# Kernel optimization log

Measured on AMD Instinct MI355X. Metric: run time of the kernel, lower is better.

The kernel has to match this reference:

```python
import jax, jax.numpy as jnp
import numpy as np

H = 8          # attention heads
HID = 256      # hidden dim
C = HID // H   # per-head channels
N = 50000      # nodes per node type
E = 500000     # edges per edge type
LRELU_SLOPE = 0.2
EPS_SOFTMAX = 1e-16
EPS_LN = 1e-5


def _gat(x_src, x_dst, ei, W, a_s, a_d, b, n_dst):
    # PyG GATConv (shared lin for src/dst since in_channels is int), concat heads
    h_src = (x_src @ W).reshape(-1, H, C)   # (Nsrc, H, C)
    h_dst = (x_dst @ W).reshape(-1, H, C)   # (Ndst, H, C)
    al_s = (h_src * a_s).sum(-1)            # (Nsrc, H)
    al_d = (h_dst * a_d).sum(-1)            # (Ndst, H)
    src, dst = ei[0], ei[1]
    alpha = jax.nn.leaky_relu(al_s[src] + al_d[dst], LRELU_SLOPE)  # (E, H)
    # segment softmax over edges grouped by destination node
    amax = jax.ops.segment_max(alpha, dst, num_segments=n_dst)
    amax = jnp.where(jnp.isfinite(amax), amax, 0.0)
    ex = jnp.exp(alpha - amax[dst])
    den = jax.ops.segment_sum(ex, dst, num_segments=n_dst)
    w = ex / (den[dst] + EPS_SOFTMAX)
    msg = h_src[src] * w[:, :, None]        # (E, H, C)
    out = jax.ops.segment_sum(msg, dst, num_segments=n_dst)
    return out.reshape(n_dst, HID) + b


def _ln(x, g, b):
    mu = x.mean(-1, keepdims=True)
    var = x.var(-1, keepdims=True)
    return (x - mu) / jnp.sqrt(var + EPS_LN) * g + b


def setup_inputs() -> dict:
    key = jax.random.key(0)
    ks = jax.random.split(key, 24)
    s = 1.0 / np.sqrt(HID)
    d = {}
    d["x_gene"] = jax.random.normal(ks[0], (N, HID), jnp.float32)
    d["x_pheno"] = jax.random.normal(ks[1], (N, HID), jnp.float32)
    d["ei_gp"] = jax.random.randint(ks[2], (2, E), 0, N, jnp.int32)
    d["ei_pg"] = jax.random.randint(ks[3], (2, E), 0, N, jnp.int32)
    d["ei_gg"] = jax.random.randint(ks[4], (2, E), 0, N, jnp.int32)
    i = 5
    for tag in ["gp", "pg", "gg"]:
        d[f"W_{tag}"] = jax.random.normal(ks[i], (HID, HID), jnp.float32) * s; i += 1
        d[f"a_s_{tag}"] = jax.random.normal(ks[i], (H, C), jnp.float32) * s; i += 1
        d[f"a_d_{tag}"] = jax.random.normal(ks[i], (H, C), jnp.float32) * s; i += 1
        d[f"b_{tag}"] = jnp.zeros((HID,), jnp.float32); i += 1
    d["ln_g_gene"] = jnp.ones((HID,), jnp.float32)
    d["ln_b_gene"] = jnp.zeros((HID,), jnp.float32)
    d["ln_g_ph"] = jnp.ones((HID,), jnp.float32)
    d["ln_b_ph"] = jnp.zeros((HID,), jnp.float32)
    return d


def reference(x_gene, x_pheno, ei_gp, ei_pg, ei_gg,
              W_gp, a_s_gp, a_d_gp, b_gp,
              W_pg, a_s_pg, a_d_pg, b_pg,
              W_gg, a_s_gg, a_d_gg, b_gg,
              ln_g_gene, ln_b_gene, ln_g_ph, ln_b_ph):
    # HeteroConv aggr='sum': sum conv outputs per destination node type
    out_gene = (_gat(x_pheno, x_gene, ei_pg, W_pg, a_s_pg, a_d_pg, b_pg, N)
                + _gat(x_gene, x_gene, ei_gg, W_gg, a_s_gg, a_d_gg, b_gg, N))
    out_ph = _gat(x_gene, x_pheno, ei_gp, W_gp, a_s_gp, a_d_gp, b_gp, N)
    # residual + layernorm (dropout is identity in eval / p=0)
    out_gene = _ln(out_gene + x_gene, ln_g_gene, ln_b_gene)
    out_ph = _ln(out_ph + x_pheno, ln_g_ph, ln_b_ph)
    return (out_gene, out_ph)
```

## Files before the change

kernel.cpp:

```cpp
#include <hip/hip_runtime.h>

#define NN 50000
#define EE 500000
#define CAP 64

typedef unsigned int u32;
typedef unsigned short ushort;
typedef __attribute__((ext_vector_type(8))) short short8v;
typedef __attribute__((ext_vector_type(4))) float float4v;

__device__ __forceinline__ ushort f2b(float f) {
  u32 u = __float_as_uint(f);
  u32 r = (u + 0x7fffu + ((u >> 16) & 1u)) >> 16;
  return (ushort)r;
}
__device__ __forceinline__ u32 pk2(float a, float b) {
  return (u32)f2b(a) | ((u32)f2b(b) << 16);
}
__device__ __forceinline__ float bl(u32 q) { return __uint_as_float(q << 16); }
__device__ __forceinline__ float bh(u32 q) { return __uint_as_float(q & 0xffff0000u); }
__device__ __forceinline__ void gload16(const void* g, void* l) {
  __builtin_amdgcn_global_load_lds((const __attribute__((address_space(1))) void*)g,
                                   (__attribute__((address_space(3))) void*)l, 16, 0, 0);
}

__global__ void prep_kernel(const float* __restrict__ W_gp, const float* __restrict__ W_pg,
                            const float* __restrict__ W_gg,
                            const float* __restrict__ as_gp, const float* __restrict__ as_pg,
                            const float* __restrict__ as_gg,
                            const float* __restrict__ ad_gp, const float* __restrict__ ad_pg,
                            const float* __restrict__ ad_gg,
                            const float* __restrict__ xg, const float* __restrict__ xp,
                            const int* __restrict__ e0, const int* __restrict__ e1,
                            const int* __restrict__ e2,
                            ushort* __restrict__ WT, ushort* __restrict__ V6T,
                            ushort* __restrict__ xb, int* __restrict__ cnt3,
                            ushort* __restrict__ srcs3) {
  int b = blockIdx.x;
  int k = threadIdx.x;
  if (b < 256) {
    int n = b;
    WT[(size_t)0 * 65536 + n * 256 + k] = f2b(W_gp[k * 256 + n]);
    WT[(size_t)1 * 65536 + n * 256 + k] = f2b(W_pg[k * 256 + n]);
    WT[(size_t)2 * 65536 + n * 256 + k] = f2b(W_gg[k * 256 + n]);
    return;
  }
  if (b < 304) {
    int idx = b - 256;
    int g = idx >> 3, h = idx & 7;
    const float* W;
    const float* a;
    switch (g) {
      case 0: W = W_gp; a = as_gp; break;
      case 1: W = W_gg; a = as_gg; break;
      case 2: W = W_pg; a = ad_pg; break;
      case 3: W = W_gg; a = ad_gg; break;
      case 4: W = W_pg; a = as_pg; break;
      default: W = W_gp; a = ad_gp; break;
    }
    const float4* wrow = (const float4*)&W[(size_t)k * 256 + h * 32];
    const float4* arow = (const float4*)&a[h * 32];
    float s = 0.f;
#pragma unroll
    for (int q = 0; q < 8; ++q) {
      float4 wv = wrow[q];
      float4 av = arow[q];
      s += wv.x * av.x + wv.y * av.y + wv.z * av.z + wv.w * av.w;
    }
    V6T[(size_t)(g * 8 + h) * 256 + k] = f2b(s);
    return;
  }
  if (b == 304) {
#pragma unroll
    for (int col = 48; col < 64; ++col) V6T[(size_t)col * 256 + k] = 0;
    return;
  }
  if (b < 2353) {
    int i = (b - 305) * 256 + k;
    const int gstride = 2048 * 256;
    const int tot = 2 * NN * 64;
    for (; i < tot; i += gstride) {
      const float* src = (i < NN * 64) ? xg + (size_t)i * 4 : xp + ((size_t)i - (size_t)NN * 64) * 4;
      float4 v = *(const float4*)src;
      ushort4 o;
      o.x = f2b(v.x); o.y = f2b(v.y); o.z = f2b(v.z); o.w = f2b(v.w);
      *(ushort4*)&xb[(size_t)i * 4] = o;
    }
    return;
  }
  int i = (b - 2353) * 256 + k;
  if (i >= 3 * EE) return;
  int which = i >= 2 * EE ? 2 : (i >= EE ? 1 : 0);
  const int* ei = which == 0 ? e0 : (which == 1 ? e1 : e2);
  int e = i - which * EE;
  int d = ei[EE + e];
  int s = ei[e];
  int gslot = which * NN + d;
  int pos = atomicAdd(&cnt3[gslot], 1);
  if (pos < CAP) srcs3[(size_t)gslot * CAP + pos] = (ushort)s;
}

__global__ __launch_bounds__(256) void compute_kernel(
    const ushort* __restrict__ xb, const ushort* __restrict__ WT,
    const ushort* __restrict__ V6T, ushort* __restrict__ hb3,
    ushort* __restrict__ alsb, float* __restrict__ ald3) {
  __shared__ ushort smem[16384];
  const int tid = threadIdx.x;
  const int l = tid & 63, w = tid >> 6;
  const int rr = l & 15, kb = l >> 4;
  if (blockIdx.y < 6) {
    ushort* As = smem;
    ushort* Bs = smem + 8192;
    const int yy = blockIdx.y;
    const int p = yy >> 1;
    const int c0 = (yy & 1) * 128;
    const ushort* x = xb + (p == 1 ? (size_t)NN * 256 : 0);
    const ushort* Wp = WT + (size_t)p * 65536 + (size_t)c0 * 256;
    ushort* hb = hb3 + (size_t)p * 12800000;
    const int r0 = blockIdx.x * 128;
    const int wm = w >> 1, wn = w & 1;
    float4v acc[4][4];
#pragma unroll
    for (int mi = 0; mi < 4; ++mi)
#pragma unroll
      for (int ni = 0; ni < 4; ++ni) acc[mi][ni] = (float4v){0.f, 0.f, 0.f, 0.f};
    const int r1 = tid >> 2, g1 = tid & 3;
    const int r2 = 64 + (tid >> 2), g2 = tid & 3;

#define STAGE(buf, k0)                                                               \
  {                                                                                  \
    gload16(&x[(size_t)(r0 + r1) * 256 + (k0) + g1 * 8], &As[(buf) * 4096 + tid * 8]); \
    gload16(&x[(size_t)(r0 + r2) * 256 + (k0) + g2 * 8], &As[(buf) * 4096 + (tid + 256) * 8]); \
    gload16(&Wp[(size_t)r1 * 256 + (k0) + g1 * 8], &Bs[(buf) * 4096 + tid * 8]);     \
    gload16(&Wp[(size_t)r2 * 256 + (k0) + g2 * 8], &Bs[(buf) * 4096 + (tid + 256) * 8]); \
  }

    STAGE(0, 0);
    __syncthreads();
#pragma unroll
    for (int k = 0; k < 8; ++k) {
      const int buf = k & 1;
      if (k < 7) STAGE(buf ^ 1, (k + 1) * 32);
      short8v af[4], bf[4];
#pragma unroll
      for (int t = 0; t < 4; ++t) {
        af[t] = *(const short8v*)&As[buf * 4096 + (wm * 64 + t * 16 + rr) * 32 + kb * 8];
        bf[t] = *(const short8v*)&Bs[buf * 4096 + (wn * 64 + t * 16 + rr) * 32 + kb * 8];
      }
#pragma unroll
      for (int mi = 0; mi < 4; ++mi)
#pragma unroll
        for (int ni = 0; ni < 4; ++ni)
          acc[mi][ni] = __builtin_amdgcn_mfma_f32_16x16x32_bf16(bf[ni], af[mi], acc[mi][ni], 0, 0, 0);
      __syncthreads();
    }
#undef STAGE
#pragma unroll
    for (int mi = 0; mi < 4; ++mi) {
      const int row = r0 + wm * 64 + mi * 16 + rr;
      if (row < NN) {
        ushort* hp = &hb[(size_t)row * 256 + c0 + wn * 64 + kb * 4];
#pragma unroll
        for (int ni = 0; ni < 4; ++ni) {
          uint2 o;
          o.x = pk2(acc[mi][ni][0], acc[mi][ni][1]);
          o.y = pk2(acc[mi][ni][2], acc[mi][ni][3]);
          *(uint2*)&hp[ni * 16] = o;
        }
      }
    }
    return;
  }
  ushort* As2 = smem;
  short8v bfv[8];
#pragma unroll
  for (int k = 0; k < 8; ++k) {
    uint4 q = *(const uint4*)&V6T[(size_t)(w * 16 + rr) * 256 + k * 32 + kb * 8];
    bfv[k] = *(short8v*)&q;
  }
  for (int t = 0; t < 4; ++t) {
    const int r0 = blockIdx.x * 256 + t * 64;
    gload16(&xb[(size_t)(r0 + (tid >> 2)) * 256 + (tid & 3) * 8], &As2[tid * 8]);
    __syncthreads();
    float4v acc[4];
#pragma unroll
    for (int mi = 0; mi < 4; ++mi) acc[mi] = (float4v){0.f, 0.f, 0.f, 0.f};
#pragma unroll
    for (int k = 0; k < 8; ++k) {
      const int buf = k & 1;
      if (k < 7)
        gload16(&xb[(size_t)(r0 + (tid >> 2)) * 256 + (k + 1) * 32 + (tid & 3) * 8],
                &As2[(buf ^ 1) * 2048 + tid * 8]);
#pragma unroll
      for (int mi = 0; mi < 4; ++mi) {
        short8v afv = *(const short8v*)&As2[buf * 2048 + (mi * 16 + rr) * 32 + kb * 8];
        acc[mi] = __builtin_amdgcn_mfma_f32_16x16x32_bf16(bfv[k], afv, acc[mi], 0, 0, 0);
      }
      __syncthreads();
    }
    const int g = w * 2 + (kb >> 1);
    const int idx = (kb & 1) * 4;
#pragma unroll
    for (int mi = 0; mi < 4; ++mi) {
      int grow = r0 + mi * 16 + rr;
      float4 val = make_float4(acc[mi][0], acc[mi][1], acc[mi][2], acc[mi][3]);
      if (grow < NN) {
        if (g == 0 || g == 1) {
          ushort* arr = alsb + (g == 0 ? 0 : 800000);
          uint2 o;
          o.x = pk2(val.x, val.y);
          o.y = pk2(val.z, val.w);
          *(uint2*)&arr[(size_t)grow * 8 + idx] = o;
        } else if (g == 2 || g == 3) {
          float* arr = ald3 + (g == 2 ? 400000 : 800000);
          *(float4*)&arr[(size_t)grow * 8 + idx] = val;
        }
      } else if (grow < 2 * NN) {
        int r = grow - NN;
        if (g == 4) {
          uint2 o;
          o.x = pk2(val.x, val.y);
          o.y = pk2(val.z, val.w);
          *(uint2*)&alsb[400000 + (size_t)r * 8 + idx] = o;
        } else if (g == 5) {
          *(float4*)&ald3[(size_t)r * 8 + idx] = val;
        }
      }
    }
  }
}

__global__ __launch_bounds__(256) void gat_gather_ln(
    const int* __restrict__ cnt3, const ushort* __restrict__ srcs3,
    const ushort* __restrict__ hb3, const ushort* __restrict__ alsb,
    const float* __restrict__ ald3, const ushort* __restrict__ xb,
    const float* __restrict__ b_gp, const float* __restrict__ b_pg,
    const float* __restrict__ b_gg,
    const float* __restrict__ lng_g, const float* __restrict__ lnb_g,
    const float* __restrict__ lng_p, const float* __restrict__ lnb_p,
    float* __restrict__ out) {
  __shared__ float exs[4][8][68];
  __shared__ int ssrc[4][64];
  const int l = threadIdx.x & 63;
  const int wv = threadIdx.x >> 6;
  const int slot = blockIdx.x * 4 + wv;
  if (slot >= 2 * NN) return;
  const bool gene = (slot < NN);
  const int d = gene ? slot : slot - NN;
  const int sl = l & 31;
  const int half = l >> 5;
  const int hh = sl >> 2;
  float vout[8] = {0.f, 0.f, 0.f, 0.f, 0.f, 0.f, 0.f, 0.f};
  const int nph = gene ? 2 : 1;
  for (int q = 0; q < nph; ++q) {
    const int phase = gene ? (1 + q) : 0;
    const int cslot = phase * NN + d;
    const ushort* hmat = hb3 + (size_t)phase * 12800000;
    const ushort* al_s = alsb + (size_t)phase * 400000;
    const float* al_d = ald3 + (size_t)phase * 400000;
    const int cnt = cnt3[cslot];
    if (cnt == 0) continue;
    const ushort* srow = srcs3 + (size_t)cslot * CAP;
    float4 ad0 = *(const float4*)&al_d[(size_t)d * 8];
    float4 ad1 = *(const float4*)&al_d[(size_t)d * 8 + 4];
    const float ald[8] = {ad0.x, ad0.y, ad0.z, ad0.w, ad1.x, ad1.y, ad1.z, ad1.w};
    float den = 0.f;
    float acc8[8] = {0.f, 0.f, 0.f, 0.f, 0.f, 0.f, 0.f, 0.f};
    const ushort* hrow = hmat + sl * 8;
    {
      float ex[8] = {0.f, 0.f, 0.f, 0.f, 0.f, 0.f, 0.f, 0.f};
      int s = 0;
      if (l < cnt) {
        s = srow[l];
        uint4 sq = *(const uint4*)&al_s[(size_t)s * 8];
        float a[8] = {bl(sq.x) + ald[0], bh(sq.x) + ald[1], bl(sq.y) + ald[2], bh(sq.y) + ald[3],
                      bl(sq.z) + ald[4], bh(sq.z) + ald[5], bl(sq.w) + ald[6], bh(sq.w) + ald[7]};
#pragma unroll
        for (int h = 0; h < 8; ++h) ex[h] = __expf(fmaxf(a[h], 0.2f * a[h]));
      }
      ssrc[wv][l] = s;
#pragma unroll
      for (int h = 0; h < 8; ++h) exs[wv][h][l] = ex[h];
      int chunkr = (cnt + 3) & ~3;
      for (int j = 0; j < chunkr; j += 4) {
        int ja = j + half, jb = j + 2 + half;
        int sa = ssrc[wv][ja], sb = ssrc[wv][jb];
        float wa = exs[wv][hh][ja], wb = exs[wv][hh][jb];
        uint4 pa = *(const uint4*)&hrow[(size_t)sa * 256];
        uint4 pb = *(const uint4*)&hrow[(size_t)sb * 256];
        den += wa + wb;
        acc8[0] += bl(pa.x) * wa + bl(pb.x) * wb;
        acc8[1] += bh(pa.x) * wa + bh(pb.x) * wb;
        acc8[2] += bl(pa.y) * wa + bl(pb.y) * wb;
        acc8[3] += bh(pa.y) * wa + bh(pb.y) * wb;
        acc8[4] += bl(pa.z) * wa + bl(pb.z) * wb;
        acc8[5] += bh(pa.z) * wa + bh(pb.z) * wb;
        acc8[6] += bl(pa.w) * wa + bl(pb.w) * wb;
        acc8[7] += bh(pa.w) * wa + bh(pb.w) * wb;
      }
    }
#pragma unroll
    for (int i = 0; i < 8; ++i) acc8[i] += __shfl_xor(acc8[i], 32);
    den += __shfl_xor(den, 32);
    float wd = 1.f / (den + 1e-16f);
#pragma unroll
    for (int i = 0; i < 8; ++i) vout[i] += acc8[i] * wd;
  }
  const ushort* xrow = xb + (gene ? 0 : (size_t)NN * 256) + (size_t)d * 256;
  uint4 xq = *(const uint4*)&xrow[sl * 8];
  float4 ba, bb;
  if (gene) {
    float4 p1 = *(const float4*)&b_pg[sl * 8];
    float4 p2 = *(const float4*)&b_pg[sl * 8 + 4];
    float4 q1 = *(const float4*)&b_gg[sl * 8];
    float4 q2 = *(const float4*)&b_gg[sl * 8 + 4];
    ba = make_float4(p1.x + q1.x, p1.y + q1.y, p1.z + q1.z, p1.w + q1.w);
    bb = make_float4(p2.x + q2.x, p2.y + q2.y, p2.z + q2.z, p2.w + q2.w);
  } else {
    ba = *(const float4*)&b_gp[sl * 8];
    bb = *(const float4*)&b_gp[sl * 8 + 4];
  }
  vout[0] += bl(xq.x) + ba.x; vout[1] += bh(xq.x) + ba.y;
  vout[2] += bl(xq.y) + ba.z; vout[3] += bh(xq.y) + ba.w;
  vout[4] += bl(xq.z) + bb.x; vout[5] += bh(xq.z) + bb.y;
  vout[6] += bl(xq.w) + bb.z; vout[7] += bh(xq.w) + bb.w;
  float s = 0.f, ss = 0.f;
#pragma unroll
  for (int i = 0; i < 8; ++i) { s += vout[i]; ss += vout[i] * vout[i]; }
#pragma unroll
  for (int off = 1; off < 32; off <<= 1) {
    s += __shfl_xor(s, off);
    ss += __shfl_xor(ss, off);
  }
  float mu = s * (1.f / 256.f);
  float var = ss * (1.f / 256.f) - mu * mu;
  float rstd = rsqrtf(var + 1e-5f);
  const float* lg = gene ? lng_g : lng_p;
  const float* lb = gene ? lnb_g : lnb_p;
  float4 g1 = *(const float4*)&lg[sl * 8];
  float4 g2 = *(const float4*)&lg[sl * 8 + 4];
  float4 c1 = *(const float4*)&lb[sl * 8];
  float4 c2 = *(const float4*)&lb[sl * 8 + 4];
  if (half == 0) {
    float* op = &out[(size_t)slot * 256 + sl * 8];
    float4 o1 = make_float4((vout[0] - mu) * rstd * g1.x + c1.x,
                            (vout[1] - mu) * rstd * g1.y + c1.y,
                            (vout[2] - mu) * rstd * g1.z + c1.z,
                            (vout[3] - mu) * rstd * g1.w + c1.w);
    float4 o2 = make_float4((vout[4] - mu) * rstd * g2.x + c2.x,
                            (vout[5] - mu) * rstd * g2.y + c2.y,
                            (vout[6] - mu) * rstd * g2.z + c2.z,
                            (vout[7] - mu) * rstd * g2.w + c2.w);
    *(float4*)op = o1;
    *(float4*)(op + 4) = o2;
  }
}

extern "C" void kernel_launch(void* const* d_in, const int* in_sizes, int n_in,
                              void* d_out, int out_size, void* d_ws, size_t ws_size,
                              hipStream_t stream) {
  const float* x_gene = (const float*)d_in[0];
  const float* x_pheno = (const float*)d_in[1];
  const int* ei_gp = (const int*)d_in[2];
  const int* ei_pg = (const int*)d_in[3];
  const int* ei_gg = (const int*)d_in[4];
  const float* W_gp = (const float*)d_in[5];
  const float* a_s_gp = (const float*)d_in[6];
  const float* a_d_gp = (const float*)d_in[7];
  const float* b_gp = (const float*)d_in[8];
  const float* W_pg = (const float*)d_in[9];
  const float* a_s_pg = (const float*)d_in[10];
  const float* a_d_pg = (const float*)d_in[11];
  const float* b_pg = (const float*)d_in[12];
  const float* W_gg = (const float*)d_in[13];
  const float* a_s_gg = (const float*)d_in[14];
  const float* a_d_gg = (const float*)d_in[15];
  const float* b_gg = (const float*)d_in[16];
  const float* ln_g_gene = (const float*)d_in[17];
  const float* ln_b_gene = (const float*)d_in[18];
  const float* ln_g_ph = (const float*)d_in[19];
  const float* ln_b_ph = (const float*)d_in[20];
  float* out = (float*)d_out;

  float* ws = (float*)d_ws;
  ushort* hb3 = (ushort*)ws;
  ushort* xb = (ushort*)(ws + 19200000);
  ushort* alsb = (ushort*)(ws + 32060000);
  float* ald3 = ws + 32700000;
  ushort* WT = (ushort*)(ws + 33960000);
  ushort* V6T = (ushort*)(ws + 34060000);
  int* ibase = (int*)(ws + 34080000);
  int* cnt3 = ibase;
  ushort* srcs3 = (ushort*)(ibase + 150016);

  const int e3blk = (3 * EE + 255) / 256;

  hipMemsetAsync(cnt3, 0, 150016 * 4, stream);
  prep_kernel<<<2353 + e3blk, 256, 0, stream>>>(
      W_gp, W_pg, W_gg, a_s_gp, a_s_pg, a_s_gg, a_d_gp, a_d_pg, a_d_gg,
      x_gene, x_pheno, ei_gp, ei_pg, ei_gg, WT, V6T, xb, cnt3, srcs3);

  compute_kernel<<<dim3(391, 7), 256, 0, stream>>>(xb, WT, V6T, hb3, alsb, ald3);

  gat_gather_ln<<<(2 * NN + 3) / 4, 256, 0, stream>>>(
      cnt3, srcs3, hb3, alsb, ald3, xb, b_gp, b_pg, b_gg,
      ln_g_gene, ln_b_gene, ln_g_ph, ln_b_ph, out);
}
```

Before: 336.5 us.

## Defer pg/gg edge bucketing into a kernel shared with pheno gather

Edge bucketing for the pg and gg edge types moves out of the prep kernel. It now runs in a new kernel whose other blocks do the pheno-node gather, which needs only the gp buckets. Gene-node gathering moves to a separate final kernel. The aim is to shorten prep and overlap the atomic bucketing with independent gather work, at the cost of one more kernel launch.

```diff
diff --git a/kernel.cpp b/kernel.cpp
--- a/kernel.cpp
+++ b/kernel.cpp
@@ -31,8 +31,7 @@
                             const float* __restrict__ ad_gp, const float* __restrict__ ad_pg,
                             const float* __restrict__ ad_gg,
                             const float* __restrict__ xg, const float* __restrict__ xp,
-                            const int* __restrict__ e0, const int* __restrict__ e1,
-                            const int* __restrict__ e2,
+                            const int* __restrict__ e0,
                             ushort* __restrict__ WT, ushort* __restrict__ V6T,
                             ushort* __restrict__ xb, int* __restrict__ cnt3,
                             ushort* __restrict__ srcs3) {
@@ -89,15 +88,11 @@
     return;
   }
   int i = (b - 2353) * 256 + k;
-  if (i >= 3 * EE) return;
-  int which = i >= 2 * EE ? 2 : (i >= EE ? 1 : 0);
-  const int* ei = which == 0 ? e0 : (which == 1 ? e1 : e2);
-  int e = i - which * EE;
-  int d = ei[EE + e];
-  int s = ei[e];
-  int gslot = which * NN + d;
-  int pos = atomicAdd(&cnt3[gslot], 1);
-  if (pos < CAP) srcs3[(size_t)gslot * CAP + pos] = (ushort)s;
+  if (i >= EE) return;
+  int d = e0[EE + i];
+  int s = e0[i];
+  int pos = atomicAdd(&cnt3[d], 1);
+  if (pos < CAP) srcs3[(size_t)d * CAP + pos] = (ushort)s;
 }
 
 __global__ __launch_bounds__(256) void compute_kernel(
@@ -230,7 +225,8 @@
   }
 }
 
-__global__ __launch_bounds__(256) void gat_gather_ln(
+__device__ __forceinline__ void gather_one(
+    int slot, int l, float* exw , int* ssw ,
     const int* __restrict__ cnt3, const ushort* __restrict__ srcs3,
     const ushort* __restrict__ hb3, const ushort* __restrict__ alsb,
     const float* __restrict__ ald3, const ushort* __restrict__ xb,
@@ -239,12 +235,6 @@
     const float* __restrict__ lng_g, const float* __restrict__ lnb_g,
     const float* __restrict__ lng_p, const float* __restrict__ lnb_p,
     float* __restrict__ out) {
-  __shared__ float exs[4][8][68];
-  __shared__ int ssrc[4][64];
-  const int l = threadIdx.x & 63;
-  const int wv = threadIdx.x >> 6;
-  const int slot = blockIdx.x * 4 + wv;
-  if (slot >= 2 * NN) return;
   const bool gene = (slot < NN);
   const int d = gene ? slot : slot - NN;
   const int sl = l & 31;
@@ -278,14 +268,14 @@
 #pragma unroll
         for (int h = 0; h < 8; ++h) ex[h] = __expf(fmaxf(a[h], 0.2f * a[h]));
       }
-      ssrc[wv][l] = s;
-#pragma unroll
-      for (int h = 0; h < 8; ++h) exs[wv][h][l] = ex[h];
+      ssw[l] = s;
+#pragma unroll
+      for (int h = 0; h < 8; ++h) exw[h * 68 + l] = ex[h];
       int chunkr = (cnt + 3) & ~3;
       for (int j = 0; j < chunkr; j += 4) {
         int ja = j + half, jb = j + 2 + half;
-        int sa = ssrc[wv][ja], sb = ssrc[wv][jb];
-        float wa = exs[wv][hh][ja], wb = exs[wv][hh][jb];
+        int sa = ssw[ja], sb = ssw[jb];
+        float wa = exw[hh * 68 + ja], wb = exw[hh * 68 + jb];
         uint4 pa = *(const uint4*)&hrow[(size_t)sa * 256];
         uint4 pb = *(const uint4*)&hrow[(size_t)sb * 256];
         den += wa + wb;
@@ -320,13 +310,12 @@
     ba = *(const float4*)&b_gp[sl * 8];
     bb = *(const float4*)&b_gp[sl * 8 + 4];
   }
-  vout[0] += bl(xq.x) + ba.x; vout[1] += bh(xq.x) + ba.y;
-  vout[2] += bl(xq.y) + ba.z; vout[3] += bh(xq.y) + ba.w;
-  vout[4] += bl(xq.z) + bb.x; vout[5] += bh(xq.z) + bb.y;
-  vout[6] += bl(xq.w) + bb.z; vout[7] += bh(xq.w) + bb.w;
-  float s = 0.f, ss = 0.f;
-#pragma unroll
-  for (int i = 0; i < 8; ++i) { s += vout[i]; ss += vout[i] * vout[i]; }
+  float v0 = vout[0] + bl(xq.x) + ba.x, v1 = vout[1] + bh(xq.x) + ba.y;
+  float v2 = vout[2] + bl(xq.y) + ba.z, v3 = vout[3] + bh(xq.y) + ba.w;
+  float v4 = vout[4] + bl(xq.z) + bb.x, v5 = vout[5] + bh(xq.z) + bb.y;
+  float v6 = vout[6] + bl(xq.w) + bb.z, v7 = vout[7] + bh(xq.w) + bb.w;
+  float s = v0 + v1 + v2 + v3 + v4 + v5 + v6 + v7;
+  float ss = v0 * v0 + v1 * v1 + v2 * v2 + v3 * v3 + v4 * v4 + v5 * v5 + v6 * v6 + v7 * v7;
 #pragma unroll
   for (int off = 1; off < 32; off <<= 1) {
     s += __shfl_xor(s, off);
@@ -343,17 +332,67 @@
   float4 c2 = *(const float4*)&lb[sl * 8 + 4];
   if (half == 0) {
     float* op = &out[(size_t)slot * 256 + sl * 8];
-    float4 o1 = make_float4((vout[0] - mu) * rstd * g1.x + c1.x,
-                            (vout[1] - mu) * rstd * g1.y + c1.y,
-                            (vout[2] - mu) * rstd * g1.z + c1.z,
-                            (vout[3] - mu) * rstd * g1.w + c1.w);
-    float4 o2 = make_float4((vout[4] - mu) * rstd * g2.x + c2.x,
-                            (vout[5] - mu) * rstd * g2.y + c2.y,
-                            (vout[6] - mu) * rstd * g2.z + c2.z,
-                            (vout[7] - mu) * rstd * g2.w + c2.w);
+    float4 o1 = make_float4((v0 - mu) * rstd * g1.x + c1.x, (v1 - mu) * rstd * g1.y + c1.y,
+                            (v2 - mu) * rstd * g1.z + c1.z, (v3 - mu) * rstd * g1.w + c1.w);
+    float4 o2 = make_float4((v4 - mu) * rstd * g2.x + c2.x, (v5 - mu) * rstd * g2.y + c2.y,
+                            (v6 - mu) * rstd * g2.z + c2.z, (v7 - mu) * rstd * g2.w + c2.w);
     *(float4*)op = o1;
     *(float4*)(op + 4) = o2;
   }
+}
+
+#define NPERM ((2 * EE + 255) / 256)
+
+__global__ __launch_bounds__(256) void perm_gather_ph(
+    const int* __restrict__ e1, const int* __restrict__ e2,
+    int* __restrict__ cnt3, ushort* __restrict__ srcs3,
+    const ushort* __restrict__ hb3, const ushort* __restrict__ alsb,
+    const float* __restrict__ ald3, const ushort* __restrict__ xb,
+    const float* __restrict__ b_gp, const float* __restrict__ b_pg,
+    const float* __restrict__ b_gg,
+    const float* __restrict__ lng_g, const float* __restrict__ lnb_g,
+    const float* __restrict__ lng_p, const float* __restrict__ lnb_p,
+    float* __restrict__ out) {
+  __shared__ float exs[4][8][68];
+  __shared__ int ssrc[4][64];
+  if (blockIdx.x < NPERM) {
+    int i = blockIdx.x * 256 + threadIdx.x;
+    if (i >= 2 * EE) return;
+    int which = (i >= EE) ? 2 : 1;
+    const int* ei = (which == 1) ? e1 : e2;
+    int e = i - (which - 1) * EE;
+    int d = ei[EE + e];
+    int s = ei[e];
+    int gslot = which * NN + d;
+    int pos = atomicAdd(&cnt3[gslot], 1);
+    if (pos < CAP) srcs3[(size_t)gslot * CAP + pos] = (ushort)s;
+    return;
+  }
+  const int l = threadIdx.x & 63;
+  const int wv = threadIdx.x >> 6;
+  int slot = NN + (blockIdx.x - NPERM) * 4 + wv;
+  if (slot >= 2 * NN) return;
+  gather_one(slot, l, &exs[wv][0][0], ssrc[wv], cnt3, srcs3, hb3, alsb, ald3, xb,
+             b_gp, b_pg, b_gg, lng_g, lnb_g, lng_p, lnb_p, out);
+}
+
+__global__ __launch_bounds__(256) void gather_gene(
+    const int* __restrict__ cnt3, const ushort* __restrict__ srcs3,
+    const ushort* __restrict__ hb3, const ushort* __restrict__ alsb,
+    const float* __restrict__ ald3, const ushort* __restrict__ xb,
+    const float* __restrict__ b_gp, const float* __restrict__ b_pg,
+    const float* __restrict__ b_gg,
+    const float* __restrict__ lng_g, const float* __restrict__ lnb_g,
+    const float* __restrict__ lng_p, const float* __restrict__ lnb_p,
+    float* __restrict__ out) {
+  __shared__ float exs[4][8][68];
+  __shared__ int ssrc[4][64];
+  const int l = threadIdx.x & 63;
+  const int wv = threadIdx.x >> 6;
+  int slot = blockIdx.x * 4 + wv;
+  if (slot >= NN) return;
+  gather_one(slot, l, &exs[wv][0][0], ssrc[wv], cnt3, srcs3, hb3, alsb, ald3, xb,
+             b_gp, b_pg, b_gg, lng_g, lnb_g, lng_p, lnb_p, out);
 }
 
 extern "C" void kernel_launch(void* const* d_in, const int* in_sizes, int n_in,
@@ -393,16 +432,20 @@
   int* cnt3 = ibase;
   ushort* srcs3 = (ushort*)(ibase + 150016);
 
-  const int e3blk = (3 * EE + 255) / 256;
+  const int egpblk = (EE + 255) / 256;
 
   hipMemsetAsync(cnt3, 0, 150016 * 4, stream);
-  prep_kernel<<<2353 + e3blk, 256, 0, stream>>>(
+  prep_kernel<<<2353 + egpblk, 256, 0, stream>>>(
       W_gp, W_pg, W_gg, a_s_gp, a_s_pg, a_s_gg, a_d_gp, a_d_pg, a_d_gg,
-      x_gene, x_pheno, ei_gp, ei_pg, ei_gg, WT, V6T, xb, cnt3, srcs3);
+      x_gene, x_pheno, ei_gp, WT, V6T, xb, cnt3, srcs3);
 
   compute_kernel<<<dim3(391, 7), 256, 0, stream>>>(xb, WT, V6T, hb3, alsb, ald3);
 
-  gat_gather_ln<<<(2 * NN + 3) / 4, 256, 0, stream>>>(
+  perm_gather_ph<<<NPERM + 12500, 256, 0, stream>>>(
+      ei_pg, ei_gg, cnt3, srcs3, hb3, alsb, ald3, xb, b_gp, b_pg, b_gg,
+      ln_g_gene, ln_b_gene, ln_g_ph, ln_b_ph, out);
+
+  gather_gene<<<12500, 256, 0, stream>>>(
       cnt3, srcs3, hb3, alsb, ald3, xb, b_gp, b_pg, b_gg,
       ln_g_gene, ln_b_gene, ln_g_ph, ln_b_ph, out);
 }
```

Measured after the change: 329.1 us. 1.02x faster.
